# Kernel optimization log

Hardware: AMD Instinct MI355X
Metric: run time of the kernel (lower is better)

## Reference

```python
import jax, jax.numpy as jnp
import numpy as np

N_HEADS = 16
D_HEAD = 64


def setup_inputs() -> dict:
    key = jax.random.key(0)
    ks = jax.random.split(key, 9)
    B, L, D = 2, 2048, 1024
    s = 0.02  # small init scale for weights
    return {
        "x": jax.random.normal(ks[0], (B, L, D), jnp.float32),
        "Wq": jax.random.normal(ks[1], (D, D), jnp.float32) * s,
        "bq": jax.random.normal(ks[2], (D,), jnp.float32) * s,
        "Wk": jax.random.normal(ks[3], (D, D), jnp.float32) * s,
        "bk": jax.random.normal(ks[4], (D,), jnp.float32) * s,
        "Wv": jax.random.normal(ks[5], (D, D), jnp.float32) * s,
        "bv": jax.random.normal(ks[6], (D,), jnp.float32) * s,
        "Wo": jax.random.normal(ks[7], (D, D), jnp.float32) * s,
        "bo": jax.random.normal(ks[8], (D,), jnp.float32) * s,
    }


def _alibi_bias(L, n_heads, dtype):
    # slopes m_i = 1 / x**(i+1), x = (2**8)**(1/n_heads)
    x = (2.0 ** 8) ** (1.0 / n_heads)
    slopes = jnp.asarray([1.0 / x ** (i + 1) for i in range(n_heads)], dtype=dtype)
    pos = jnp.arange(L)
    rel = (pos[None, :] - pos[:, None]).astype(dtype)  # [L, L], (j - i)
    return slopes[:, None, None] * rel[None, :, :]      # [H, L, L]


def reference(x, Wq, bq, Wk, bk, Wv, bv, Wo, bo):
    B, L, D = x.shape
    H, dh = N_HEADS, D_HEAD
    scale = dh ** -0.5
    q = (x @ Wq + bq).reshape(B, L, H, dh)
    k = (x @ Wk + bk).reshape(B, L, H, dh)
    v = (x @ Wv + bv).reshape(B, L, H, dh)
    scores = jnp.einsum("blhd,bmhd->bhlm", q, k) * scale  # [B,H,L,L]
    bias = _alibi_bias(L, H, scores.dtype)                 # [H,L,L]
    attn = jax.nn.softmax(scores + bias[None], axis=-1)
    out = jnp.einsum("bhlm,bmhd->blhd", attn, v).reshape(B, L, D)
    return out @ Wo + bo
```

## Files before the change

### kernel.cpp

```cpp
#include <hip/hip_runtime.h>
#include <cstdint>
#include <cstddef>

typedef unsigned short u16;
typedef unsigned int u32;
typedef __bf16 bf16x8 __attribute__((ext_vector_type(8)));
typedef float f32x4 __attribute__((ext_vector_type(4)));
typedef u32 u32x4 __attribute__((ext_vector_type(4)));
typedef u32 u32x2 __attribute__((ext_vector_type(2)));
typedef unsigned short u16x8 __attribute__((ext_vector_type(8)));
typedef short s16x4 __attribute__((ext_vector_type(4)));

#if __has_builtin(__builtin_amdgcn_mfma_f32_16x16x16bf16_1k)
#define HAVE_MFMA16 1
#else
#define HAVE_MFMA16 0
#endif

__device__ __forceinline__ u16 f2bf(float f) {
    u32 u = __float_as_uint(f);
    u += 0x7fffu + ((u >> 16) & 1u);
    return (u16)(u >> 16);
}

__device__ __forceinline__ float fexp2(float x) {
    float r;
    asm("v_exp_f32 %0, %1" : "=v"(r) : "v"(x));
    return r;
}

__device__ __forceinline__ void gl16(const void* g, void* l) {
    __builtin_amdgcn_global_load_lds(
        (const __attribute__((address_space(1))) unsigned int*)g,
        (__attribute__((address_space(3))) unsigned int*)l, 16, 0, 0);
}

__global__ __launch_bounds__(256) void cvt_x_k(const float* __restrict__ x,
                                               u16* __restrict__ o) {
    int i = blockIdx.x * 256 + threadIdx.x;
    const float4* xv = (const float4*)x;
    float4 a = xv[2 * i], b = xv[2 * i + 1];
    ushort4 r0, r1;
    r0.x = f2bf(a.x); r0.y = f2bf(a.y); r0.z = f2bf(a.z); r0.w = f2bf(a.w);
    r1.x = f2bf(b.x); r1.y = f2bf(b.y); r1.z = f2bf(b.z); r1.w = f2bf(b.w);
    ((ushort4*)o)[2 * i] = r0;
    ((ushort4*)o)[2 * i + 1] = r1;
}

__global__ __launch_bounds__(256) void cvt_wT4_k(const float* __restrict__ Wq,
                                                 const float* __restrict__ Wk,
                                                 const float* __restrict__ Wv,
                                                 const float* __restrict__ Wo,
                                                 u16* __restrict__ oqkv,
                                                 u16* __restrict__ oo) {
    __shared__ float tile[64][65];
    const int z = blockIdx.z;
    const float* W = (z == 0) ? Wq : (z == 1) ? Wk : (z == 2) ? Wv : Wo;
    u16* o = (z < 3) ? (oqkv + ((size_t)z << 20)) : oo;
    const int bx = blockIdx.x, by = blockIdx.y;
    const int t = threadIdx.x, tn = t & 63, tr = t >> 6;
#pragma unroll
    for (int r = 0; r < 16; ++r) {
        int kk = r * 4 + tr;
        tile[kk][tn] = W[(size_t)(by * 64 + kk) * 1024 + bx * 64 + tn];
    }
    __syncthreads();
#pragma unroll
    for (int r = 0; r < 16; ++r) {
        int nn = r * 4 + tr;
        o[(size_t)(bx * 64 + nn) * 1024 + by * 64 + tn] = f2bf(tile[tn][nn]);
    }
}

template <int MODE>
__global__ __launch_bounds__(256) void gemm_k(
    const u16* __restrict__ A, const u16* __restrict__ Bt,
    const float* __restrict__ bias0, const float* __restrict__ bias1,
    const float* __restrict__ bias2,
    u16* __restrict__ oq, u16* __restrict__ ok_, u16* __restrict__ ov,
    float* __restrict__ oc) {
    __shared__ __align__(16) u16 As[3 * 128 * 32];
    __shared__ __align__(16) u16 Bs[3 * 128 * 32];
    const int t = threadIdx.x, w = t >> 6, lane = t & 63;
    const int lr = lane & 15, lg = lane >> 4;
    const int brow = blockIdx.x * 128, bcol = blockIdx.y * 128;
    const int wr = w >> 1, wc = w & 1;
    const char* Ab = (const char*)A + (size_t)brow * 2048;
    const char* Bb = (const char*)Bt + (size_t)bcol * 2048;
    const int lrow = lane >> 2;
    const int lcol = (((lane & 3) ^ ((lane >> 3) & 3)) << 4);
    const int r0a = w * 32, r0b = w * 32 + 16;
    const size_t ga = (size_t)(r0a + lrow) * 2048 + lcol;
    const size_t gb = (size_t)(r0b + lrow) * 2048 + lcol;
    const int rsw = ((lg ^ ((lr >> 1) & 3)) << 4);

    f32x4 acc[4][4];
#pragma unroll
    for (int m = 0; m < 4; ++m)
#pragma unroll
        for (int n = 0; n < 4; ++n) acc[m][n] = (f32x4){0.f, 0.f, 0.f, 0.f};

    gl16(Ab + ga, (char*)As + r0a * 64);
    gl16(Ab + gb, (char*)As + r0b * 64);
    gl16(Bb + ga, (char*)Bs + r0a * 64);
    gl16(Bb + gb, (char*)Bs + r0b * 64);
    gl16(Ab + ga + 64, (char*)As + 8192 + r0a * 64);
    gl16(Ab + gb + 64, (char*)As + 8192 + r0b * 64);
    gl16(Bb + ga + 64, (char*)Bs + 8192 + r0a * 64);
    gl16(Bb + gb + 64, (char*)Bs + 8192 + r0b * 64);

    for (int tt = 0; tt < 32; ++tt) {
        if (tt < 31) {
            asm volatile("s_waitcnt vmcnt(4)" ::: "memory");
        } else {
            asm volatile("s_waitcnt vmcnt(0)" ::: "memory");
        }
        __builtin_amdgcn_s_barrier();
        __builtin_amdgcn_sched_barrier(0);
        if (tt < 30) {
            const int nb = (tt + 2) % 3;
            const size_t ko = (size_t)(tt + 2) * 64;
            char* Asn = (char*)As + nb * 8192;
            char* Bsn = (char*)Bs + nb * 8192;
            gl16(Ab + ga + ko, Asn + r0a * 64);
            gl16(Ab + gb + ko, Asn + r0b * 64);
            gl16(Bb + ga + ko, Bsn + r0a * 64);
            gl16(Bb + gb + ko, Bsn + r0b * 64);
        }
        const char* AsB = (const char*)As + (tt % 3) * 8192;
        const char* BsB = (const char*)Bs + (tt % 3) * 8192;
        bf16x8 af[4], bfr[4];
#pragma unroll
        for (int m = 0; m < 4; ++m)
            af[m] = *(const bf16x8*)(AsB + (wr * 64 + m * 16 + lr) * 64 + rsw);
#pragma unroll
        for (int n = 0; n < 4; ++n)
            bfr[n] = *(const bf16x8*)(BsB + (wc * 64 + n * 16 + lr) * 64 + rsw);
#pragma unroll
        for (int m = 0; m < 4; ++m)
#pragma unroll
            for (int n = 0; n < 4; ++n)
                acc[m][n] = __builtin_amdgcn_mfma_f32_16x16x32_bf16(af[m], bfr[n],
                                                                    acc[m][n], 0, 0, 0);
    }

    const float QSCALE = 0.125f * 1.44269504f;
#pragma unroll
    for (int n = 0; n < 4; ++n) {
        const int col = bcol + wc * 64 + n * 16 + lr;
        if (MODE == 0) {
#pragma unroll
            for (int m = 0; m < 4; ++m)
#pragma unroll
                for (int r = 0; r < 4; ++r) {
                    int row = brow + wr * 64 + m * 16 + 4 * lg + r;
                    int b = row >> 11, l = row & 2047;
                    float val = acc[m][n][r];
                    if (col < 1024) {
                        int hh = col >> 6, d = col & 63;
                        oq[(((size_t)b * 16 + hh) * 2048 + l) * 64 + d] =
                            f2bf((val + bias0[col]) * QSCALE);
                    } else if (col < 2048) {
                        int c = col - 1024, hh = c >> 6, d = c & 63;
                        ok_[(((size_t)b * 16 + hh) * 2048 + l) * 64 + d] =
                            f2bf(val + bias1[c]);
                    } else {
                        int c = col - 2048, hh = c >> 6, d = c & 63;
                        ov[(((size_t)b * 16 + hh) * 64 + d) * 2048 + l] =
                            f2bf(val + bias2[c]);
                    }
                }
        } else {
            const float bb = bias0[col];
#pragma unroll
            for (int m = 0; m < 4; ++m)
#pragma unroll
                for (int r = 0; r < 4; ++r) {
                    int row = brow + wr * 64 + m * 16 + 4 * lg + r;
                    oc[(size_t)row * 1024 + col] = acc[m][n][r] + bb;
                }
        }
    }
}

__global__ __launch_bounds__(256, 2) void attn_k(const u16* __restrict__ qg_,
                                                 const u16* __restrict__ kg_,
                                                 const u16* __restrict__ vg_,
                                                 u16* __restrict__ ao) {
    __shared__ __align__(16) u16 smem[24576];
    char* Kbase = (char*)smem;
    char* Vbase = (char*)smem + 24576;
    const int t = threadIdx.x, w = t >> 6, lane = t & 63;
    const int lr = lane & 15, lg = lane >> 4;
    const int bid = blockIdx.y * 16 + blockIdx.x;
    const int qt = (bid >> 3) & 15;
    const int bh = ((bid >> 7) << 3) | (bid & 7);
    const int q0 = qt * 128, h = bh & 15, bb = bh >> 4;
    const float sl2 = exp2f(-0.5f * (float)(h + 1)) * 1.44269504f;

    const int U0 = (w * 2) * 64 + lane, U1 = U0 + 64;
    const int rr0 = U0 >> 3, u0 = U0 & 7, rr1 = U1 >> 3, u1 = U1 & 7;
    const int koff0 = rr0 * 128 + ((u0 ^ (rr0 & 7)) << 4);
    const int koff1 = rr1 * 128 + ((u1 ^ (rr1 & 7)) << 4);
    const int voff0 = rr0 * 4096 + ((u0 ^ (rr0 & 7)) << 4);
    const int voff1 = rr1 * 4096 + ((u1 ^ (rr1 & 7)) << 4);
    const int lds0 = (w * 2) * 1024, lds1 = lds0 + 1024;

    const char* khead = (const char*)(kg_ + (size_t)bh * 2048 * 64);
    const char* vhead = (const char*)(vg_ + (size_t)bh * 64 * 2048);

    const char* qpA = (const char*)qg_ +
                      ((size_t)bh * 2048 + q0 + w * 32 + lr) * 128;
    bf16x8 qa0A = *(const bf16x8*)(qpA + lg * 16);
    bf16x8 qa1A = *(const bf16x8*)(qpA + 64 + lg * 16);
    bf16x8 qa0B = *(const bf16x8*)(qpA + 2048 + lg * 16);
    bf16x8 qa1B = *(const bf16x8*)(qpA + 2048 + 64 + lg * 16);

    gl16(khead + koff0, Kbase + lds0);
    gl16(khead + koff1, Kbase + lds1);
    gl16(vhead + voff0, Vbase + lds0);
    gl16(vhead + voff1, Vbase + lds1);
    gl16(khead + 8192 + koff0, Kbase + 8192 + lds0);
    gl16(khead + 8192 + koff1, Kbase + 8192 + lds1);
    gl16(vhead + 128 + voff0, Vbase + 8192 + lds0);
    gl16(vhead + 128 + voff1, Vbase + 8192 + lds1);

    f32x4 abF2[4];
#pragma unroll
    for (int n = 0; n < 4; ++n)
#pragma unroll
        for (int r = 0; r < 4; ++r)
            abF2[n][r] = sl2 * (float)(n * 16 + 4 * lg + r - 2047) - 16.0f;
    const float ainc = sl2 * 64.0f;
    f32x4 oaccA[4], oaccB[4];
#pragma unroll
    for (int nn = 0; nn < 4; ++nn) {
        oaccA[nn] = (f32x4){0.f, 0.f, 0.f, 0.f};
        oaccB[nn] = (f32x4){0.f, 0.f, 0.f, 0.f};
    }
#if HAVE_MFMA16
    f32x4 laccA = (f32x4){0.f, 0.f, 0.f, 0.f};
    f32x4 laccB = (f32x4){0.f, 0.f, 0.f, 0.f};
    const u32x2 onesb = {0x3F803F80u, 0x3F803F80u};
    const s16x4 ones = __builtin_bit_cast(s16x4, onesb);
#else
    f32x4 l4A = (f32x4){0.f, 0.f, 0.f, 0.f};
    f32x4 l4B = (f32x4){0.f, 0.f, 0.f, 0.f};
    const int srcA = lr + ((lg & 1) << 5);
    const int srcB = srcA + 16;
    const bool hiHalf = (lg >> 1) != 0;
#endif

    for (int tt = 0; tt < 32; ++tt) {
        if (tt < 31) {
            asm volatile("s_waitcnt vmcnt(4)" ::: "memory");
        } else {
            asm volatile("s_waitcnt vmcnt(0)" ::: "memory");
        }
        __builtin_amdgcn_s_barrier();
        __builtin_amdgcn_sched_barrier(0);
        if (tt < 30) {
            const int nb = (tt + 2) % 3;
            const char* ks = khead + (size_t)(tt + 2) * 8192;
            const char* vs = vhead + (size_t)(tt + 2) * 128;
            gl16(ks + koff0, Kbase + nb * 8192 + lds0);
            gl16(ks + koff1, Kbase + nb * 8192 + lds1);
            gl16(vs + voff0, Vbase + nb * 8192 + lds0);
            gl16(vs + voff1, Vbase + nb * 8192 + lds1);
        }
        const char* Kc = Kbase + (tt % 3) * 8192;
        const char* Vc = Vbase + (tt % 3) * 8192;

        bf16x8 kf0[4], kf1[4];
#pragma unroll
        for (int n = 0; n < 4; ++n)
            kf0[n] = *(const bf16x8*)(Kc + (n * 16 + lr) * 128 +
                                      ((lg ^ (lr & 7)) << 4));
#pragma unroll
        for (int n = 0; n < 4; ++n)
            kf1[n] = *(const bf16x8*)(Kc + (n * 16 + lr) * 128 +
                                      (((4 + lg) ^ (lr & 7)) << 4));
#if HAVE_MFMA16
        s16x4 va_[4][4];
#pragma unroll
        for (int n = 0; n < 4; ++n)
#pragma unroll
            for (int nn = 0; nn < 4; ++nn)
                va_[n][nn] = *(const s16x4*)(Vc + (nn * 16 + lr) * 128 +
                                             (((2 * n + (lg >> 1)) ^ (lr & 7)) << 4) +
                                             ((lg & 1) << 3));
#endif

        f32x4 saA[4], saB[4];
        __builtin_amdgcn_s_setprio(1);
#pragma unroll
        for (int n = 0; n < 4; ++n) {
            saA[n] = __builtin_amdgcn_mfma_f32_16x16x32_bf16(kf0[n], qa0A, abF2[n],
                                                             0, 0, 0);
            saB[n] = __builtin_amdgcn_mfma_f32_16x16x32_bf16(kf0[n], qa0B, abF2[n],
                                                             0, 0, 0);
        }
#pragma unroll
        for (int n = 0; n < 4; ++n) {
            saA[n] = __builtin_amdgcn_mfma_f32_16x16x32_bf16(kf1[n], qa1A, saA[n],
                                                             0, 0, 0);
            saB[n] = __builtin_amdgcn_mfma_f32_16x16x32_bf16(kf1[n], qa1B, saB[n],
                                                             0, 0, 0);
        }
        __builtin_amdgcn_s_setprio(0);

#pragma unroll
        for (int n = 0; n < 4; ++n)
#pragma unroll
            for (int r = 0; r < 4; ++r) {
                saA[n][r] = fexp2(saA[n][r]);
                saB[n][r] = fexp2(saB[n][r]);
            }
#pragma unroll
        for (int n = 0; n < 4; ++n) abF2[n] += ainc;

#if HAVE_MFMA16
        s16x4 pnA[4], pnB[4];
#pragma unroll
        for (int n = 0; n < 4; ++n) {
            u32 lo, hi;
            asm("v_cvt_pk_bf16_f32 %0, %1, %2"
                : "=v"(lo) : "v"(saA[n][0]), "v"(saA[n][1]));
            asm("v_cvt_pk_bf16_f32 %0, %1, %2"
                : "=v"(hi) : "v"(saA[n][2]), "v"(saA[n][3]));
            u32x2 tmpa = {lo, hi};
            pnA[n] = __builtin_bit_cast(s16x4, tmpa);
            asm("v_cvt_pk_bf16_f32 %0, %1, %2"
                : "=v"(lo) : "v"(saB[n][0]), "v"(saB[n][1]));
            asm("v_cvt_pk_bf16_f32 %0, %1, %2"
                : "=v"(hi) : "v"(saB[n][2]), "v"(saB[n][3]));
            u32x2 tmpb = {lo, hi};
            pnB[n] = __builtin_bit_cast(s16x4, tmpb);
        }
        __builtin_amdgcn_s_setprio(1);
#pragma unroll
        for (int n = 0; n < 4; ++n) {
            laccA = __builtin_amdgcn_mfma_f32_16x16x16bf16_1k(ones, pnA[n],
                                                              laccA, 0, 0, 0);
            laccB = __builtin_amdgcn_mfma_f32_16x16x16bf16_1k(ones, pnB[n],
                                                              laccB, 0, 0, 0);
#pragma unroll
            for (int nn = 0; nn < 4; ++nn) {
                oaccA[nn] = __builtin_amdgcn_mfma_f32_16x16x16bf16_1k(va_[n][nn],
                                                                      pnA[n],
                                                                      oaccA[nn],
                                                                      0, 0, 0);
                oaccB[nn] = __builtin_amdgcn_mfma_f32_16x16x16bf16_1k(va_[n][nn],
                                                                      pnB[n],
                                                                      oaccB[nn],
                                                                      0, 0, 0);
            }
        }
        __builtin_amdgcn_s_setprio(0);
#else
#pragma unroll
        for (int n = 0; n < 4; ++n) { l4A += saA[n]; l4B += saB[n]; }
        u32 pk[8];
        u32x4 pb0, pb1;
#pragma unroll
        for (int n = 0; n < 4; ++n)
#pragma unroll
            for (int rp = 0; rp < 2; ++rp) {
                u32 rpk;
                asm("v_cvt_pk_bf16_f32 %0, %1, %2"
                    : "=v"(rpk) : "v"(saA[n][2 * rp]), "v"(saA[n][2 * rp + 1]));
                pk[n * 2 + rp] = rpk;
            }
#pragma unroll
        for (int g = 0; g < 4; ++g) {
            int src = (g < 2) ? srcA : srcB;
            u32 a0 = (u32)__shfl((int)pk[0 + (g & 1)], src);
            u32 a1 = (u32)__shfl((int)pk[2 + (g & 1)], src);
            u32 b0 = (u32)__shfl((int)pk[4 + (g & 1)], src);
            u32 b1 = (u32)__shfl((int)pk[6 + (g & 1)], src);
            pb0[g] = hiHalf ? a1 : a0;
            pb1[g] = hiHalf ? b1 : b0;
        }
        {
            bf16x8 pf0 = __builtin_bit_cast(bf16x8, pb0);
            bf16x8 pf1 = __builtin_bit_cast(bf16x8, pb1);
#pragma unroll
            for (int nn = 0; nn < 4; ++nn) {
                bf16x8 vf0 = *(const bf16x8*)(Vc + (nn * 16 + lr) * 128 +
                                              ((lg ^ (lr & 7)) << 4));
                oaccA[nn] = __builtin_amdgcn_mfma_f32_16x16x32_bf16(vf0, pf0,
                                                                    oaccA[nn], 0, 0, 0);
                bf16x8 vf1 = *(const bf16x8*)(Vc + (nn * 16 + lr) * 128 +
                                              (((4 + lg) ^ (lr & 7)) << 4));
                oaccA[nn] = __builtin_amdgcn_mfma_f32_16x16x32_bf16(vf1, pf1,
                                                                    oaccA[nn], 0, 0, 0);
            }
        }
#pragma unroll
        for (int n = 0; n < 4; ++n)
#pragma unroll
            for (int rp = 0; rp < 2; ++rp) {
                u32 rpk;
                asm("v_cvt_pk_bf16_f32 %0, %1, %2"
                    : "=v"(rpk) : "v"(saB[n][2 * rp]), "v"(saB[n][2 * rp + 1]));
                pk[n * 2 + rp] = rpk;
            }
#pragma unroll
        for (int g = 0; g < 4; ++g) {
            int src = (g < 2) ? srcA : srcB;
            u32 a0 = (u32)__shfl((int)pk[0 + (g & 1)], src);
            u32 a1 = (u32)__shfl((int)pk[2 + (g & 1)], src);
            u32 b0 = (u32)__shfl((int)pk[4 + (g & 1)], src);
            u32 b1 = (u32)__shfl((int)pk[6 + (g & 1)], src);
            pb0[g] = hiHalf ? a1 : a0;
            pb1[g] = hiHalf ? b1 : b0;
        }
        {
            bf16x8 pf0 = __builtin_bit_cast(bf16x8, pb0);
            bf16x8 pf1 = __builtin_bit_cast(bf16x8, pb1);
#pragma unroll
            for (int nn = 0; nn < 4; ++nn) {
                bf16x8 vf0 = *(const bf16x8*)(Vc + (nn * 16 + lr) * 128 +
                                              ((lg ^ (lr & 7)) << 4));
                oaccB[nn] = __builtin_amdgcn_mfma_f32_16x16x32_bf16(vf0, pf0,
                                                                    oaccB[nn], 0, 0, 0);
                bf16x8 vf1 = *(const bf16x8*)(Vc + (nn * 16 + lr) * 128 +
                                              (((4 + lg) ^ (lr & 7)) << 4));
                oaccB[nn] = __builtin_amdgcn_mfma_f32_16x16x32_bf16(vf1, pf1,
                                                                    oaccB[nn], 0, 0, 0);
            }
        }
#endif
    }

    __syncthreads();
#if HAVE_MFMA16
    const float linvA = 1.0f / laccA[0];
    const float linvB = 1.0f / laccB[0];
#else
    float lA = (l4A[0] + l4A[1]) + (l4A[2] + l4A[3]);
    lA += __shfl_xor(lA, 16);
    lA += __shfl_xor(lA, 32);
    float lB = (l4B[0] + l4B[1]) + (l4B[2] + l4B[3]);
    lB += __shfl_xor(lB, 16);
    lB += __shfl_xor(lB, 32);
    const float linvA = 1.0f / lA, linvB = 1.0f / lB;
#endif
    u16* ow = smem + w * (32 * 72);
#pragma unroll
    for (int nn = 0; nn < 4; ++nn)
#pragma unroll
        for (int r = 0; r < 4; ++r) {
            ow[lr * 72 + nn * 16 + 4 * lg + r] = f2bf(oaccA[nn][r] * linvA);
            ow[(16 + lr) * 72 + nn * 16 + 4 * lg + r] = f2bf(oaccB[nn][r] * linvB);
        }
    __syncthreads();
    const int q_ = lane >> 2, d0 = (lane & 3) << 4;
    const u16* orowA = smem + w * (32 * 72) + q_ * 72 + d0;
    const u16* orowB = orowA + 16 * 72;
    u16x8 a0 = *(const u16x8*)(orowA);
    u16x8 a1 = *(const u16x8*)(orowA + 8);
    u16x8 b0 = *(const u16x8*)(orowB);
    u16x8 b1 = *(const u16x8*)(orowB + 8);
    size_t gaddr = ((size_t)bb * 2048 + q0 + w * 32 + q_) * 1024 + h * 64 + d0;
    *(u16x8*)(ao + gaddr) = a0;
    *(u16x8*)(ao + gaddr + 8) = a1;
    *(u16x8*)(ao + gaddr + 16 * 1024) = b0;
    *(u16x8*)(ao + gaddr + 16 * 1024 + 8) = b1;
}

extern "C" void kernel_launch(void* const* d_in, const int* in_sizes, int n_in,
                              void* d_out, int out_size, void* d_ws, size_t ws_size,
                              hipStream_t stream) {
    const float* x  = (const float*)d_in[0];
    const float* Wq = (const float*)d_in[1];
    const float* bq = (const float*)d_in[2];
    const float* Wk = (const float*)d_in[3];
    const float* bk = (const float*)d_in[4];
    const float* Wv = (const float*)d_in[5];
    const float* bv = (const float*)d_in[6];
    const float* Wo = (const float*)d_in[7];
    const float* bo = (const float*)d_in[8];

    const size_t MB = 1u << 20;
    if (ws_size < 40 * MB) return;
    char* ws = (char*)d_ws;
    u16* xb    = (u16*)(ws);
    u16* wqkvt = (u16*)(ws + 8 * MB);
    u16* wot   = (u16*)(ws + 14 * MB);
    u16* qb    = (u16*)(ws + 16 * MB);
    u16* kb    = (u16*)(ws + 24 * MB);
    u16* vt    = (u16*)(ws + 32 * MB);
    u16* ao    = xb;

    cvt_x_k<<<2048, 256, 0, stream>>>(x, xb);
    cvt_wT4_k<<<dim3(16, 16, 4), 256, 0, stream>>>(Wq, Wk, Wv, Wo, wqkvt, wot);

    gemm_k<0><<<dim3(32, 24), 256, 0, stream>>>(xb, wqkvt, bq, bk, bv,
                                                qb, kb, vt, nullptr);
    attn_k<<<dim3(16, 32), 256, 0, stream>>>(qb, kb, vt, ao);
    gemm_k<1><<<dim3(32, 8), 256, 0, stream>>>(ao, wot, bo, nullptr, nullptr,
                                               nullptr, nullptr, nullptr,
                                               (float*)d_out);
}
```

Measured before the change: 125.3 us.

## Use 128x256 tiles with 512 threads for fused QKV projection GEMM

```diff
diff --git a/kernel.cpp b/kernel.cpp
--- a/kernel.cpp
+++ b/kernel.cpp
@@ -72,13 +72,103 @@
     }
 }
 
-template <int MODE>
-__global__ __launch_bounds__(256) void gemm_k(
+__global__ __launch_bounds__(512, 4) void gemm256_k(
     const u16* __restrict__ A, const u16* __restrict__ Bt,
     const float* __restrict__ bias0, const float* __restrict__ bias1,
     const float* __restrict__ bias2,
-    u16* __restrict__ oq, u16* __restrict__ ok_, u16* __restrict__ ov,
-    float* __restrict__ oc) {
+    u16* __restrict__ oq, u16* __restrict__ ok_, u16* __restrict__ ov) {
+    __shared__ __align__(16) u16 As[3 * 128 * 32];
+    __shared__ __align__(16) u16 Bs[3 * 256 * 32];
+    const int t = threadIdx.x, w = t >> 6, lane = t & 63;
+    const int lr = lane & 15, lg = lane >> 4;
+    const int brow = blockIdx.x * 128, bcol = blockIdx.y * 256;
+    const int wr = w >> 2, wc = w & 3;
+    const char* Ab = (const char*)A + (size_t)brow * 2048;
+    const char* Bb = (const char*)Bt + (size_t)bcol * 2048;
+    const int lrow = lane >> 2;
+    const int lcol = (((lane & 3) ^ ((lane >> 3) & 3)) << 4);
+    const size_t gaA = (size_t)(w * 16 + lrow) * 2048 + lcol;
+    const size_t gaB0 = (size_t)(w * 32 + lrow) * 2048 + lcol;
+    const size_t gaB1 = (size_t)(w * 32 + 16 + lrow) * 2048 + lcol;
+    const int dA = w * 1024, dB0 = w * 2048, dB1 = w * 2048 + 1024;
+    const int rsw = ((lg ^ ((lr >> 1) & 3)) << 4);
+
+    f32x4 acc[4][4];
+#pragma unroll
+    for (int m = 0; m < 4; ++m)
+#pragma unroll
+        for (int n = 0; n < 4; ++n) acc[m][n] = (f32x4){0.f, 0.f, 0.f, 0.f};
+
+    gl16(Ab + gaA, (char*)As + dA);
+    gl16(Bb + gaB0, (char*)Bs + dB0);
+    gl16(Bb + gaB1, (char*)Bs + dB1);
+    gl16(Ab + gaA + 64, (char*)As + 8192 + dA);
+    gl16(Bb + gaB0 + 64, (char*)Bs + 16384 + dB0);
+    gl16(Bb + gaB1 + 64, (char*)Bs + 16384 + dB1);
+
+    for (int tt = 0; tt < 32; ++tt) {
+        if (tt < 31) {
+            asm volatile("s_waitcnt vmcnt(3)" ::: "memory");
+        } else {
+            asm volatile("s_waitcnt vmcnt(0)" ::: "memory");
+        }
+        __builtin_amdgcn_s_barrier();
+        __builtin_amdgcn_sched_barrier(0);
+        if (tt < 30) {
+            const int nb = (tt + 2) % 3;
+            const size_t ko = (size_t)(tt + 2) * 64;
+            gl16(Ab + gaA + ko, (char*)As + nb * 8192 + dA);
+            gl16(Bb + gaB0 + ko, (char*)Bs + nb * 16384 + dB0);
+            gl16(Bb + gaB1 + ko, (char*)Bs + nb * 16384 + dB1);
+        }
+        const char* AsB = (const char*)As + (tt % 3) * 8192;
+        const char* BsB = (const char*)Bs + (tt % 3) * 16384;
+        bf16x8 af[4], bfr[4];
+#pragma unroll
+        for (int m = 0; m < 4; ++m)
+            af[m] = *(const bf16x8*)(AsB + (wr * 64 + m * 16 + lr) * 64 + rsw);
+#pragma unroll
+        for (int n = 0; n < 4; ++n)
+            bfr[n] = *(const bf16x8*)(BsB + (wc * 64 + n * 16 + lr) * 64 + rsw);
+#pragma unroll
+        for (int m = 0; m < 4; ++m)
+#pragma unroll
+            for (int n = 0; n < 4; ++n)
+                acc[m][n] = __builtin_amdgcn_mfma_f32_16x16x32_bf16(af[m], bfr[n],
+                                                                    acc[m][n], 0, 0, 0);
+    }
+
+    const float QSCALE = 0.125f * 1.44269504f;
+#pragma unroll
+    for (int n = 0; n < 4; ++n) {
+        const int col = bcol + wc * 64 + n * 16 + lr;
+#pragma unroll
+        for (int m = 0; m < 4; ++m)
+#pragma unroll
+            for (int r = 0; r < 4; ++r) {
+                int row = brow + wr * 64 + m * 16 + 4 * lg + r;
+                int b = row >> 11, l = row & 2047;
+                float val = acc[m][n][r];
+                if (col < 1024) {
+                    int hh = col >> 6, d = col & 63;
+                    oq[(((size_t)b * 16 + hh) * 2048 + l) * 64 + d] =
+                        f2bf((val + bias0[col]) * QSCALE);
+                } else if (col < 2048) {
+                    int c = col - 1024, hh = c >> 6, d = c & 63;
+                    ok_[(((size_t)b * 16 + hh) * 2048 + l) * 64 + d] =
+                        f2bf(val + bias1[c]);
+                } else {
+                    int c = col - 2048, hh = c >> 6, d = c & 63;
+                    ov[(((size_t)b * 16 + hh) * 64 + d) * 2048 + l] =
+                        f2bf(val + bias2[c]);
+                }
+            }
+    }
+}
+
+__global__ __launch_bounds__(256) void gemm_k(
+    const u16* __restrict__ A, const u16* __restrict__ Bt,
+    const float* __restrict__ bias0, float* __restrict__ oc) {
     __shared__ __align__(16) u16 As[3 * 128 * 32];
     __shared__ __align__(16) u16 Bs[3 * 128 * 32];
     const int t = threadIdx.x, w = t >> 6, lane = t & 63;
@@ -144,42 +234,17 @@
                                                                     acc[m][n], 0, 0, 0);
     }
 
-    const float QSCALE = 0.125f * 1.44269504f;
 #pragma unroll
     for (int n = 0; n < 4; ++n) {
         const int col = bcol + wc * 64 + n * 16 + lr;
-        if (MODE == 0) {
-#pragma unroll
-            for (int m = 0; m < 4; ++m)
-#pragma unroll
-                for (int r = 0; r < 4; ++r) {
-                    int row = brow + wr * 64 + m * 16 + 4 * lg + r;
-                    int b = row >> 11, l = row & 2047;
-                    float val = acc[m][n][r];
-                    if (col < 1024) {
-                        int hh = col >> 6, d = col & 63;
-                        oq[(((size_t)b * 16 + hh) * 2048 + l) * 64 + d] =
-                            f2bf((val + bias0[col]) * QSCALE);
-                    } else if (col < 2048) {
-                        int c = col - 1024, hh = c >> 6, d = c & 63;
-                        ok_[(((size_t)b * 16 + hh) * 2048 + l) * 64 + d] =
-                            f2bf(val + bias1[c]);
-                    } else {
-                        int c = col - 2048, hh = c >> 6, d = c & 63;
-                        ov[(((size_t)b * 16 + hh) * 64 + d) * 2048 + l] =
-                            f2bf(val + bias2[c]);
-                    }
-                }
-        } else {
-            const float bb = bias0[col];
-#pragma unroll
-            for (int m = 0; m < 4; ++m)
-#pragma unroll
-                for (int r = 0; r < 4; ++r) {
-                    int row = brow + wr * 64 + m * 16 + 4 * lg + r;
-                    oc[(size_t)row * 1024 + col] = acc[m][n][r] + bb;
-                }
-        }
+        const float bb = bias0[col];
+#pragma unroll
+        for (int m = 0; m < 4; ++m)
+#pragma unroll
+            for (int r = 0; r < 4; ++r) {
+                int row = brow + wr * 64 + m * 16 + 4 * lg + r;
+                oc[(size_t)row * 1024 + col] = acc[m][n][r] + bb;
+            }
     }
 }
 
@@ -496,10 +561,8 @@
     cvt_x_k<<<2048, 256, 0, stream>>>(x, xb);
     cvt_wT4_k<<<dim3(16, 16, 4), 256, 0, stream>>>(Wq, Wk, Wv, Wo, wqkvt, wot);
 
-    gemm_k<0><<<dim3(32, 24), 256, 0, stream>>>(xb, wqkvt, bq, bk, bv,
-                                                qb, kb, vt, nullptr);
+    gemm256_k<<<dim3(32, 12), 512, 0, stream>>>(xb, wqkvt, bq, bk, bv,
+                                                qb, kb, vt);
     attn_k<<<dim3(16, 32), 256, 0, stream>>>(qb, kb, vt, ao);
-    gemm_k<1><<<dim3(32, 8), 256, 0, stream>>>(ao, wot, bo, nullptr, nullptr,
-                                               nullptr, nullptr, nullptr,
-                                               (float*)d_out);
-}
+    gemm_k<<<dim3(32, 8), 256, 0, stream>>>(ao, wot, bo, (float*)d_out);
+}
```

Result: slower. 133.5 us (+6.6%).
